# Kernel tuning notes

Hardware: AMD Instinct MI355X
Metric: run time of the kernel (lower is better)

The kernel has to match this reference:

```python
import jax, jax.numpy as jnp
import numpy as np

# Model hyperparameters (from __init__)
SIGMA = 0.2
LAMBDA_0 = 1.0
LAMBDA_INF = 0.1
LAMBDA_DECAY = 0.01
MU_J = 0.0
SIGMA_J = 0.3
TOTAL_STEPS = 10000
KAPPA = float(np.exp(MU_J + 0.5 * SIGMA_J ** 2) - 1.0)  # E[e^Y - 1]

# Simulation dims (simulate_path args)
T_TOTAL = 1.0
N_STEPS = 2048
N_PATHS = 32768
DT = T_TOTAL / N_STEPS


def _jump_intensity(t):
    # lambda(t) = lambda_inf + (lambda_0 - lambda_inf) * exp(-decay * t)
    # (t/total_steps * total_steps cancels in the original code)
    return LAMBDA_INF + (LAMBDA_0 - LAMBDA_INF) * jnp.exp(-LAMBDA_DECAY * t)


def setup_inputs() -> dict:
    key = jax.random.key(0)
    k1, k2, k3 = jax.random.split(key, 3)
    # Per-step time-varying Poisson rate for jump counts
    t = jnp.arange(N_STEPS, dtype=jnp.float32) * DT  # (n_steps,)
    lam_dt = _jump_intensity(t) * DT                  # (n_steps,)
    n_jumps = jax.random.poisson(k3, lam_dt[:, None], shape=(N_STEPS, N_PATHS)).astype(jnp.int32)
    return {
        "S0": jnp.ones((1,), dtype=jnp.float32),                         # initial price
        "z_diff": jax.random.normal(k1, (N_STEPS, N_PATHS), jnp.float32),  # Brownian increments / sqrt(dt)
        "z_jump": jax.random.normal(k2, (N_STEPS, N_PATHS), jnp.float32),  # jump-sum normals
        "n_jumps": n_jumps,                                              # Poisson jump counts
    }


def reference(S0, z_diff, z_jump, n_jumps):
    dtype = z_diff.dtype
    t = jnp.arange(N_STEPS, dtype=dtype) * DT          # (n_steps,)
    lam = _jump_intensity(t)[:, None]                   # (n_steps, 1)
    # Sum of n_jumps iid N(mu_J, sigma_J^2) jumps == N(n*mu_J, n*sigma_J^2)
    nj = n_jumps.astype(dtype)
    jump_sizes = nj * MU_J + jnp.sqrt(nj) * SIGMA_J * z_jump
    drift = (0.0 - lam * KAPPA) * DT
    diffusion = SIGMA * jnp.asarray(np.sqrt(DT), dtype) * z_diff
    log_ret = drift + diffusion + jump_sizes            # (n_steps, n_paths)
    log_paths = jnp.cumsum(log_ret, axis=0)             # (n_steps, n_paths)
    log_paths = jnp.concatenate([jnp.zeros((1, log_ret.shape[1]), dtype), log_paths], axis=0)
    paths = (S0[0] * jnp.exp(log_paths)).T              # (n_paths, n_steps + 1)
    return paths
```

## Files before the change

### kernel.cpp

```cpp
#include <hip/hip_runtime.h>
#include <math.h>


#define N_STEPS 2048
#define N_PATHS 32768
#define ROW (N_STEPS + 1)

#define NWAVES 16
#define SUB 8
#define TILE_S (NWAVES * SUB)
#define NTILES (N_STEPS / TILE_S)

#define DT_F 0.00048828125f
#define C_DIFF_F 0.004419417382415922f
#define KAPPA_F 0.046027859908717f
#define ND_F (-4.8828125e-6f)

__global__ __launch_bounds__(1024, 4) void merton_paths_kernel(
    const float* __restrict__ S0,
    const float* __restrict__ z_diff,
    const float* __restrict__ z_jump,
    const int* __restrict__ n_jumps,
    float* __restrict__ out) {
    const int tid  = threadIdx.x;
    const int lane = tid & 63;
    const int w    = tid >> 6;
    const int pbase = blockIdx.x * 64;
    const int p     = pbase + lane;
    const float s0  = S0[0];

    __shared__ float stage[64][TILE_S + 1];
    __shared__ float ws[NWAVES][64];

    const float r = __expf(ND_F);

    if (w == 0) out[(size_t)p * ROW] = s0;

    const float* zd_p = z_diff  + (size_t)(w * SUB) * N_PATHS + p;
    const float* zj_p = z_jump  + (size_t)(w * SUB) * N_PATHS + p;
    const int*   nj_p = n_jumps + (size_t)(w * SUB) * N_PATHS + p;

    float carry = 0.0f;

    for (int t = 0; t < NTILES; ++t) {
        float zd[SUB], zj[SUB];
        int   nj[SUB];
#pragma unroll
        for (int i = 0; i < SUB; ++i) {
            size_t off = (size_t)i * N_PATHS;
            zd[i] = zd_p[off];
            zj[i] = zj_p[off];
            nj[i] = nj_p[off];
        }
        float e = __expf(ND_F * (float)(t * TILE_S + w * SUB));
        float c[SUB];
        float acc = 0.0f;
#pragma unroll
        for (int i = 0; i < SUB; ++i) {
            float lam = 0.1f + 0.9f * e;
            e *= r;
            float drift = -(lam * KAPPA_F) * DT_F;
            float njf = (float)nj[i];
            float val = (drift + C_DIFF_F * zd[i]) + sqrtf(njf) * 0.3f * zj[i];
            acc += val;
            c[i] = acc;
        }
        ws[w][lane] = acc;
        __syncthreads();

        float pre = carry;
        float tot = 0.0f;
#pragma unroll
        for (int ww = 0; ww < NWAVES; ++ww) {
            float v = ws[ww][lane];
            pre += (ww < w) ? v : 0.0f;
            tot += v;
        }
        carry += tot;

#pragma unroll
        for (int i = 0; i < SUB; ++i) {
            stage[lane][w * SUB + i] = s0 * __expf(pre + c[i]);
        }
        __syncthreads();

        {
            float* obase = out + (size_t)pbase * ROW + 1 + t * TILE_S;
#pragma unroll
            for (int k = 0; k < 4; ++k) {
                int rr = w * 4 + k;
                float* orow = obase + (size_t)rr * ROW;
                orow[lane]      = stage[rr][lane];
                orow[lane + 64] = stage[rr][lane + 64];
            }
        }
        __syncthreads();

        zd_p += (size_t)TILE_S * N_PATHS;
        zj_p += (size_t)TILE_S * N_PATHS;
        nj_p += (size_t)TILE_S * N_PATHS;
    }
}

extern "C" void kernel_launch(void* const* d_in, const int* in_sizes, int n_in,
                              void* d_out, int out_size, void* d_ws, size_t ws_size,
                              hipStream_t stream) {
    const float* S0      = (const float*)d_in[0];
    const float* z_diff  = (const float*)d_in[1];
    const float* z_jump  = (const float*)d_in[2];
    const int*   n_jumps = (const int*)d_in[3];
    float* out = (float*)d_out;

    dim3 block(1024);
    dim3 grid(N_PATHS / 64);
    hipLaunchKernelGGL(merton_paths_kernel, grid, block, 0, stream,
                       S0, z_diff, z_jump, n_jumps, out);
}
```

Before: 840.4 us.

## Prefetch next tile's inputs and double-buffer staging to drop a barrier

Each iteration now issues the global loads for the next tile's z_diff, z_jump and n_jumps before the current tile's scan and output. The per-element log-returns are computed after the stores, so load latency can overlap with LDS work and global writes. The staging buffer becomes double-buffered, which removes the trailing __syncthreads; the remaining barriers use a raw s_waitcnt plus s_barrier. Indexing switches to 32-bit and the launch-bounds occupancy hint rises from 4 to 8, which tightens register limits and risks spills given the extra live prefetch registers.

```diff
diff --git a/kernel.cpp b/kernel.cpp
--- a/kernel.cpp
+++ b/kernel.cpp
@@ -16,7 +16,12 @@
 #define KAPPA_F 0.046027859908717f
 #define ND_F (-4.8828125e-6f)
 
-__global__ __launch_bounds__(1024, 4) void merton_paths_kernel(
+__device__ __forceinline__ void lds_barrier() {
+    asm volatile("s_waitcnt lgkmcnt(0)" ::: "memory");
+    __builtin_amdgcn_s_barrier();
+}
+
+__global__ __launch_bounds__(1024, 8) void merton_paths_kernel(
     const float* __restrict__ S0,
     const float* __restrict__ z_diff,
     const float* __restrict__ z_jump,
@@ -29,47 +34,57 @@
     const int p     = pbase + lane;
     const float s0  = S0[0];
 
-    __shared__ float stage[64][TILE_S + 1];
+    __shared__ float stage[2][64][TILE_S + 1];
     __shared__ float ws[NWAVES][64];
 
     const float r = __expf(ND_F);
 
-    if (w == 0) out[(size_t)p * ROW] = s0;
+    if (w == 0) out[p * ROW] = s0;
 
-    const float* zd_p = z_diff  + (size_t)(w * SUB) * N_PATHS + p;
-    const float* zj_p = z_jump  + (size_t)(w * SUB) * N_PATHS + p;
-    const int*   nj_p = n_jumps + (size_t)(w * SUB) * N_PATHS + p;
+    float zd[SUB], zj[SUB], val[SUB];
+    int   nj[SUB];
+
+    {
+        int idx = (w * SUB) * N_PATHS + p;
+#pragma unroll
+        for (int i = 0; i < SUB; ++i) {
+            zd[i] = z_diff[idx];
+            zj[i] = z_jump[idx];
+            nj[i] = n_jumps[idx];
+            idx += N_PATHS;
+        }
+        float e = __expf(ND_F * (float)(w * SUB));
+#pragma unroll
+        for (int i = 0; i < SUB; ++i) {
+            float lam = 0.1f + 0.9f * e;
+            e *= r;
+            val[i] = (-(lam * KAPPA_F) * DT_F + C_DIFF_F * zd[i])
+                   + sqrtf((float)nj[i]) * 0.3f * zj[i];
+        }
+    }
 
     float carry = 0.0f;
 
     for (int t = 0; t < NTILES; ++t) {
-        float zd[SUB], zj[SUB];
-        int   nj[SUB];
+        const int tn = (t + 1 < NTILES) ? (t + 1) : 0;
+        {
+            int idx = (tn * TILE_S + w * SUB) * N_PATHS + p;
 #pragma unroll
-        for (int i = 0; i < SUB; ++i) {
-            size_t off = (size_t)i * N_PATHS;
-            zd[i] = zd_p[off];
-            zj[i] = zj_p[off];
-            nj[i] = nj_p[off];
+            for (int i = 0; i < SUB; ++i) {
+                zd[i] = z_diff[idx];
+                zj[i] = z_jump[idx];
+                nj[i] = n_jumps[idx];
+                idx += N_PATHS;
+            }
         }
-        float e = __expf(ND_F * (float)(t * TILE_S + w * SUB));
-        float c[SUB];
+
         float acc = 0.0f;
 #pragma unroll
-        for (int i = 0; i < SUB; ++i) {
-            float lam = 0.1f + 0.9f * e;
-            e *= r;
-            float drift = -(lam * KAPPA_F) * DT_F;
-            float njf = (float)nj[i];
-            float val = (drift + C_DIFF_F * zd[i]) + sqrtf(njf) * 0.3f * zj[i];
-            acc += val;
-            c[i] = acc;
-        }
+        for (int i = 0; i < SUB; ++i) { acc += val[i]; val[i] = acc; }
         ws[w][lane] = acc;
-        __syncthreads();
+        lds_barrier();
 
-        float pre = carry;
-        float tot = 0.0f;
+        float pre = carry, tot = 0.0f;
 #pragma unroll
         for (int ww = 0; ww < NWAVES; ++ww) {
             float v = ws[ww][lane];
@@ -78,27 +93,31 @@
         }
         carry += tot;
 
+        const int buf = t & 1;
 #pragma unroll
-        for (int i = 0; i < SUB; ++i) {
-            stage[lane][w * SUB + i] = s0 * __expf(pre + c[i]);
-        }
-        __syncthreads();
+        for (int i = 0; i < SUB; ++i)
+            stage[buf][lane][w * SUB + i] = s0 * __expf(pre + val[i]);
+        lds_barrier();
 
         {
-            float* obase = out + (size_t)pbase * ROW + 1 + t * TILE_S;
+            float* obase = out + pbase * ROW + 1 + t * TILE_S;
 #pragma unroll
             for (int k = 0; k < 4; ++k) {
                 int rr = w * 4 + k;
-                float* orow = obase + (size_t)rr * ROW;
-                orow[lane]      = stage[rr][lane];
-                orow[lane + 64] = stage[rr][lane + 64];
+                float* orow = obase + rr * ROW;
+                orow[lane]      = stage[buf][rr][lane];
+                orow[lane + 64] = stage[buf][rr][lane + 64];
             }
         }
-        __syncthreads();
 
-        zd_p += (size_t)TILE_S * N_PATHS;
-        zj_p += (size_t)TILE_S * N_PATHS;
-        nj_p += (size_t)TILE_S * N_PATHS;
+        float e = __expf(ND_F * (float)(tn * TILE_S + w * SUB));
+#pragma unroll
+        for (int i = 0; i < SUB; ++i) {
+            float lam = 0.1f + 0.9f * e;
+            e *= r;
+            val[i] = (-(lam * KAPPA_F) * DT_F + C_DIFF_F * zd[i])
+                   + sqrtf((float)nj[i]) * 0.3f * zj[i];
+        }
     }
 }
 
```

Result: no change. 843.6 us (+0.4%).
